# Kernel optimization log

Measured on AMD Instinct MI355X. Metric: run time of the kernel, lower is better.

Reference implementation:

```python
import jax, jax.numpy as jnp
import numpy as np

IN_FEATURES = 8192
OUT_FEATURES = 28672


def setup_inputs() -> dict:
    key = jax.random.key(0)
    k1, k2, k3, k4 = jax.random.split(key, 4)
    x = jax.random.normal(k1, (1, IN_FEATURES), dtype=jnp.float32)
    # packed int4 codes: two 4-bit codes per uint8 byte (low nibble = even col, high nibble = odd col)
    qweight = jax.random.randint(k2, (OUT_FEATURES, IN_FEATURES // 2), 0, 256, dtype=jnp.int32).astype(jnp.uint8)
    # per-output-row 16-entry codebook (K-means values), indexed by the 4-bit code
    kmvalues = jax.random.normal(k3, (OUT_FEATURES, 16), dtype=jnp.float32)
    bias = jax.random.normal(k4, (OUT_FEATURES,), dtype=jnp.float32) * 0.01
    return {"x": x, "qweight": qweight, "kmvalues": kmvalues, "bias": bias}


def reference(x, qweight, kmvalues, bias):
    # Unpack two 4-bit codes per byte; matches pack_to_i4: byte = lo | (hi << 4)
    lo = (qweight & 0xF).astype(jnp.int32)   # even columns
    hi = (qweight >> 4).astype(jnp.int32)    # odd columns
    codes = jnp.stack([lo, hi], axis=-1).reshape(qweight.shape[0], -1)  # (O, I)
    # Dequantize via per-row 16-entry lookup table
    W = jnp.take_along_axis(kmvalues, codes, axis=1)  # (O, I) float32
    # Single-token matvec: y = x @ W^T + bias
    y = x @ W.T + bias  # (1, O)
    return y
```

## Files before the change

kernel.cpp:

```cpp
#include <hip/hip_runtime.h>
#include <stdint.h>


typedef _Float16 half2_t __attribute__((ext_vector_type(2)));

#define OUT_F     28672
#define ROW_ELEMS 4096
#define NBLOCKS   1024
#define WPB       4
#define NWAVES    (NBLOCKS * WPB)
#define RPW       (OUT_F / NWAVES)

__device__ __forceinline__ float dot2acc(half2_t a, half2_t b, float c) {
#if __has_builtin(__builtin_amdgcn_fdot2)
    return __builtin_amdgcn_fdot2(a, b, c, false);
#else
    return c + (float)a.x * (float)b.x + (float)a.y * (float)b.y;
#endif
}

__global__ __launch_bounds__(256) void q4lut_matvec(
    const float* __restrict__ x,
    const int*   __restrict__ qw,
    const float* __restrict__ kmv,
    const float* __restrict__ bias,
    float* __restrict__ out)
{
    __shared__ uint32_t pairlut[WPB][256];

    const int tid   = threadIdx.x;
    const int wave  = tid >> 6;
    const int lane  = tid & 63;
    const int gwave = blockIdx.x * WPB + wave;

    half2_t xp[64];
#pragma unroll
    for (int c = 0; c < 16; ++c) {
        const float4* xs = reinterpret_cast<const float4*>(x + c * 512 + lane * 8);
        float4 v0 = xs[0];
        float4 v1 = xs[1];
        xp[c * 4 + 0] = half2_t{(_Float16)v0.x, (_Float16)v0.y};
        xp[c * 4 + 1] = half2_t{(_Float16)v0.z, (_Float16)v0.w};
        xp[c * 4 + 2] = half2_t{(_Float16)v1.x, (_Float16)v1.y};
        xp[c * 4 + 3] = half2_t{(_Float16)v1.z, (_Float16)v1.w};
    }

    for (int r = 0; r < RPW; ++r) {
        const int row = gwave + NWAVES * r;

        const uint4* qrow =
            reinterpret_cast<const uint4*>(qw + (size_t)row * ROW_ELEMS);
        uint4 cs[16];
#pragma unroll
        for (int c = 0; c < 16; ++c) cs[c] = qrow[c * 64 + lane];

        const float    myv = kmv[row * 16 + (lane & 15)];
        const _Float16 hih = (_Float16)__shfl(myv, lane >> 2, 64);
        uint32_t ent[4];
#pragma unroll
        for (int k = 0; k < 4; ++k) {
            const _Float16 loh = (_Float16)__shfl(myv, ((lane & 3) << 2) + k, 64);
            half2_t p = {loh, hih};
            ent[k] = __builtin_bit_cast(uint32_t, p);
        }
        *reinterpret_cast<uint4*>(&pairlut[wave][lane * 4]) =
            make_uint4(ent[0], ent[1], ent[2], ent[3]);

        __syncthreads();

        float acc = 0.f;
#pragma unroll
        for (int c = 0; c < 16; ++c) {
            const uint32_t dws[4] = {cs[c].x, cs[c].y, cs[c].z, cs[c].w};
#pragma unroll
            for (int k = 0; k < 4; ++k) {
                const uint32_t idx = dws[k] & 0xffu;
                const uint32_t pw  = pairlut[wave][idx];
                acc = dot2acc(xp[c * 4 + k], __builtin_bit_cast(half2_t, pw), acc);
            }
        }

#pragma unroll
        for (int off = 32; off > 0; off >>= 1)
            acc += __shfl_xor(acc, off, 64);
        if (lane == 0) out[row] = acc + bias[row];
    }
}

extern "C" void kernel_launch(void* const* d_in, const int* in_sizes, int n_in,
                              void* d_out, int out_size, void* d_ws, size_t ws_size,
                              hipStream_t stream) {
    const float* x    = (const float*)d_in[0];
    const int*   qw   = (const int*)d_in[1];
    const float* kmv  = (const float*)d_in[2];
    const float* bias = (const float*)d_in[3];
    float*       out  = (float*)d_out;

    hipLaunchKernelGGL(q4lut_matvec, dim3(NBLOCKS), dim3(256), 0, stream,
                       x, qw, kmv, bias, out);
}
```

Measured before the change: 598.8 us.

## Split each row across four waves and reduce partials in shared memory

Instead of each wave processing a full row, the four waves of a block now each handle a quarter of the row's K dimension, producing partial sums that are combined through shared memory at the end. Each block owns a contiguous set of rows (16 per block over 1792 blocks), which shrinks the per-thread x register cache from 64 to 16 half2 values and allows higher occupancy via launch bounds. The LUT is built from direct vector loads of the codebook instead of shuffles, duplicated into two copies to reduce LDS bank conflicts, and the per-row __syncthreads is removed. Dropping that barrier relies on each wave only touching its own LUT, with a possible LDS write-after-read hazard across iterations within a wave.

Result: no change. 599.6 us (+0.1%).

```diff
diff --git a/kernel.cpp b/kernel.cpp
--- a/kernel.cpp
+++ b/kernel.cpp
@@ -4,12 +4,11 @@
 
 typedef _Float16 half2_t __attribute__((ext_vector_type(2)));
 
-#define OUT_F     28672
-#define ROW_ELEMS 4096
-#define NBLOCKS   1024
-#define WPB       4
-#define NWAVES    (NBLOCKS * WPB)
-#define RPW       (OUT_F / NWAVES)
+#define OUT_F   28672
+#define ROW_E   4096
+#define QTR     1024
+#define NBLOCKS 1792
+#define RPB     (OUT_F / NBLOCKS)
 
 __device__ __forceinline__ float dot2acc(half2_t a, half2_t b, float c) {
 #if __has_builtin(__builtin_amdgcn_fdot2)
@@ -19,24 +18,28 @@
 #endif
 }
 
-__global__ __launch_bounds__(256) void q4lut_matvec(
+__global__ __launch_bounds__(256, 4) void q4lut_matvec(
     const float* __restrict__ x,
     const int*   __restrict__ qw,
     const float* __restrict__ kmv,
     const float* __restrict__ bias,
     float* __restrict__ out)
 {
-    __shared__ uint32_t pairlut[WPB][256];
+    __shared__ uint32_t pairlut[4][2][256];
+    __shared__ float    partial[RPB][4];
 
-    const int tid   = threadIdx.x;
-    const int wave  = tid >> 6;
-    const int lane  = tid & 63;
-    const int gwave = blockIdx.x * WPB + wave;
+    const int tid  = threadIdx.x;
+    const int wave = tid >> 6;
+    const int lane = tid & 63;
+    const int rowbase = blockIdx.x * RPB;
 
-    half2_t xp[64];
+    const uint32_t* lut = &pairlut[wave][lane >> 5][0];
+
+    half2_t xp[16];
 #pragma unroll
-    for (int c = 0; c < 16; ++c) {
-        const float4* xs = reinterpret_cast<const float4*>(x + c * 512 + lane * 8);
+    for (int c = 0; c < 4; ++c) {
+        const float4* xs =
+            reinterpret_cast<const float4*>(x + wave * 2048 + c * 512 + lane * 8);
         float4 v0 = xs[0];
         float4 v1 = xs[1];
         xp[c * 4 + 0] = half2_t{(_Float16)v0.x, (_Float16)v0.y};
@@ -45,45 +48,51 @@
         xp[c * 4 + 3] = half2_t{(_Float16)v1.z, (_Float16)v1.w};
     }
 
-    for (int r = 0; r < RPW; ++r) {
-        const int row = gwave + NWAVES * r;
+    for (int r = 0; r < RPB; ++r) {
+        const int row = rowbase + r;
 
-        const uint4* qrow =
-            reinterpret_cast<const uint4*>(qw + (size_t)row * ROW_ELEMS);
-        uint4 cs[16];
-#pragma unroll
-        for (int c = 0; c < 16; ++c) cs[c] = qrow[c * 64 + lane];
+        const uint4* q4 = reinterpret_cast<const uint4*>(
+            qw + (size_t)row * ROW_E + wave * QTR);
+        uint4 cs0 = q4[0 * 64 + lane];
+        uint4 cs1 = q4[1 * 64 + lane];
+        uint4 cs2 = q4[2 * 64 + lane];
+        uint4 cs3 = q4[3 * 64 + lane];
 
-        const float    myv = kmv[row * 16 + (lane & 15)];
-        const _Float16 hih = (_Float16)__shfl(myv, lane >> 2, 64);
-        uint32_t ent[4];
-#pragma unroll
-        for (int k = 0; k < 4; ++k) {
-            const _Float16 loh = (_Float16)__shfl(myv, ((lane & 3) << 2) + k, 64);
-            half2_t p = {loh, hih};
-            ent[k] = __builtin_bit_cast(uint32_t, p);
-        }
-        *reinterpret_cast<uint4*>(&pairlut[wave][lane * 4]) =
-            make_uint4(ent[0], ent[1], ent[2], ent[3]);
-
-        __syncthreads();
+        const float* kr = kmv + row * 16;
+        const float  hif = kr[lane >> 2];
+        const float4 lo4 = reinterpret_cast<const float4*>(kr)[lane & 3];
+        const _Float16 hih = (_Float16)hif;
+        uint32_t e0 = __builtin_bit_cast(uint32_t, half2_t{(_Float16)lo4.x, hih});
+        uint32_t e1 = __builtin_bit_cast(uint32_t, half2_t{(_Float16)lo4.y, hih});
+        uint32_t e2 = __builtin_bit_cast(uint32_t, half2_t{(_Float16)lo4.z, hih});
+        uint32_t e3 = __builtin_bit_cast(uint32_t, half2_t{(_Float16)lo4.w, hih});
+        uint4 ent = make_uint4(e0, e1, e2, e3);
+        *reinterpret_cast<uint4*>(&pairlut[wave][0][lane * 4]) = ent;
+        *reinterpret_cast<uint4*>(&pairlut[wave][1][lane * 4]) = ent;
 
         float acc = 0.f;
+        const uint4 cs[4] = {cs0, cs1, cs2, cs3};
 #pragma unroll
-        for (int c = 0; c < 16; ++c) {
-            const uint32_t dws[4] = {cs[c].x, cs[c].y, cs[c].z, cs[c].w};
-#pragma unroll
-            for (int k = 0; k < 4; ++k) {
-                const uint32_t idx = dws[k] & 0xffu;
-                const uint32_t pw  = pairlut[wave][idx];
-                acc = dot2acc(xp[c * 4 + k], __builtin_bit_cast(half2_t, pw), acc);
-            }
+        for (int c = 0; c < 4; ++c) {
+            const uint32_t d0 = cs[c].x, d1 = cs[c].y, d2 = cs[c].z, d3 = cs[c].w;
+            acc = dot2acc(xp[c * 4 + 0], __builtin_bit_cast(half2_t, lut[d0 & 0xffu]), acc);
+            acc = dot2acc(xp[c * 4 + 1], __builtin_bit_cast(half2_t, lut[d1 & 0xffu]), acc);
+            acc = dot2acc(xp[c * 4 + 2], __builtin_bit_cast(half2_t, lut[d2 & 0xffu]), acc);
+            acc = dot2acc(xp[c * 4 + 3], __builtin_bit_cast(half2_t, lut[d3 & 0xffu]), acc);
         }
 
 #pragma unroll
         for (int off = 32; off > 0; off >>= 1)
             acc += __shfl_xor(acc, off, 64);
-        if (lane == 0) out[row] = acc + bias[row];
+        if (lane == 0) partial[r][wave] = acc;
+    }
+
+    __syncthreads();
+
+    if (tid < RPB) {
+        const int row = rowbase + tid;
+        out[row] = partial[tid][0] + partial[tid][1] +
+                   partial[tid][2] + partial[tid][3] + bias[row];
     }
 }
 
```
